# Optimization experiments

Hardware: AMD Instinct MI355X
Metric: run time of the kernel (lower is better)

The kernel has to match this reference:

```python
import jax, jax.numpy as jnp
import numpy as np

N, F, E, FE, H, OUT = 20000, 128, 320000, 16, 128, 128
NTYPES = 2  # types = (0, 1)
NPAIRS = NTYPES * NTYPES


def setup_inputs() -> dict:
    key = jax.random.key(0)
    ks = jax.random.split(key, 12)
    edge_in_dim = 2 * F + FE
    node_in_dim = F + H
    s = lambda *shape: 1.0 / np.sqrt(shape[-2])
    return {
        "x": jax.random.normal(ks[0], (N, 1, F), dtype=jnp.float32),
        "edge_index": jax.random.randint(ks[1], (2, E), 0, N, dtype=jnp.int64),
        "edge_attr": jax.random.normal(ks[2], (E, FE), dtype=jnp.float32),
        "node_type": jax.random.randint(ks[3], (N,), 0, NTYPES, dtype=jnp.int64),
        # edge MLP params, stacked over the 4 (t1,t2) type pairs
        "ew1": jax.random.normal(ks[4], (NPAIRS, edge_in_dim, H), dtype=jnp.float32) * (1.0 / np.sqrt(edge_in_dim)),
        "eb1": jnp.zeros((NPAIRS, H), dtype=jnp.float32),
        "ew2": jax.random.normal(ks[5], (NPAIRS, H, H), dtype=jnp.float32) * (1.0 / np.sqrt(H)),
        "eb2": jnp.zeros((NPAIRS, H), dtype=jnp.float32),
        # node MLP params, stacked over the 2 node types
        "nw1": jax.random.normal(ks[6], (NTYPES, node_in_dim, H), dtype=jnp.float32) * (1.0 / np.sqrt(node_in_dim)),
        "nb1": jnp.zeros((NTYPES, H), dtype=jnp.float32),
        "nw2": jax.random.normal(ks[7], (NTYPES, H, OUT), dtype=jnp.float32) * (1.0 / np.sqrt(H)),
        "nb2": jnp.zeros((NTYPES, OUT), dtype=jnp.float32),
    }


def reference(x, edge_index, edge_attr, node_type, ew1, eb1, ew2, eb2, nw1, nb1, nw2, nb2):
    x0 = x[:, 0]  # [N, F]
    row, col = edge_index[0], edge_index[1]

    # ---- edge model: type-pair-dispatched 2-layer ReLU MLP ----
    edge_in = jnp.concatenate([x0[row], x0[col], edge_attr], axis=-1)  # [E, 2F+FE]
    h1 = jax.nn.relu(jnp.einsum("ei,pih->eph", edge_in, ew1) + eb1)    # [E, P, H]
    h2 = jax.nn.relu(jnp.einsum("eph,phk->epk", h1, ew2) + eb2)        # [E, P, H]
    pair_id = node_type[row] * NTYPES + node_type[col]                  # [E]
    pair_oh = jax.nn.one_hot(pair_id, NPAIRS, dtype=h2.dtype)           # [E, P]
    edge_feat = jnp.einsum("epk,ep->ek", h2, pair_oh)                   # [E, H]

    # ---- aggregation: sum over incoming edges per source (row) node ----
    agg = jax.ops.segment_sum(edge_feat, row, num_segments=N)           # [N, H]

    # ---- node model: type-dispatched 2-layer MLP + residual ----
    node_in = jnp.concatenate([x0, agg], axis=-1)                       # [N, F+H]
    n1 = jax.nn.relu(jnp.einsum("ni,tih->nth", node_in, nw1) + nb1)     # [N, T, H]
    n2 = jnp.einsum("nth,thk->ntk", n1, nw2) + nb2                      # [N, T, OUT]
    type_oh = jax.nn.one_hot(node_type, NTYPES, dtype=n2.dtype)         # [N, T]
    out = jnp.einsum("ntk,nt->nk", n2, type_oh)                         # [N, OUT]
    out = out + x0[:, :OUT]  # residual
    return out[:, None, :]  # [N, 1, OUT]
```

## Files before the change

kernel.cpp:

```cpp
#include <hip/hip_runtime.h>

#define N_NODES 20000
#define N_EDGES 320000
#define NBINS   (4*N_NODES)
#define SCAN_NBLK 313

typedef unsigned short u16;
typedef __attribute__((ext_vector_type(8))) short bf16x8;
typedef __attribute__((ext_vector_type(4))) float f32x4;
typedef __attribute__((ext_vector_type(4))) unsigned int u32x4;
typedef __attribute__((ext_vector_type(2))) unsigned int u32x2;

__device__ __forceinline__ float b2f(u16 b){
  unsigned u = ((unsigned)b) << 16; float f; __builtin_memcpy(&f, &u, 4); return f;
}
__device__ __forceinline__ u16 f2b(float f){
  unsigned u; __builtin_memcpy(&u, &f, 4); u += 0x7FFF + ((u >> 16) & 1); return (u16)(u >> 16);
}
__device__ __forceinline__ unsigned cvtpk(float a, float b){
  unsigned r;
  asm("v_cvt_pk_bf16_f32 %0, %1, %2" : "=v"(r) : "v"(a), "v"(b));
  return r;
}

#define NX   (N_NODES*128)
#define NW1T (4*288*128)
#define NW2T (4*128*128)
#define NN1  (2*256*128)
#define NN2  (2*128*128)

__global__ void k_preconv(const float* __restrict__ x,
                          const float* __restrict__ ew1, const float* __restrict__ ew2,
                          const float* __restrict__ nw1, const float* __restrict__ nw2,
                          u16* __restrict__ x0b,
                          u16* __restrict__ wt1t, u16* __restrict__ wt2t,
                          u16* __restrict__ nw1t, u16* __restrict__ nw2t)
{
  int t = blockIdx.x * 256 + threadIdx.x;
  if (t < NX) { x0b[t] = f2b(x[t]); return; }
  t -= NX;
  if (t < NW1T) {
    int p = t / 36864, r = t % 36864; int k = r >> 7, n = r & 127;
    float v = (k < 272) ? ew1[(p * 272 + k) * 128 + n] : 0.f;
    wt1t[(p * 128 + n) * 288 + k] = f2b(v);
    return;
  }
  t -= NW1T;
  if (t < NW2T) {
    int p = t >> 14, r = t & 16383; int k = r >> 7, n = r & 127;
    wt2t[(p * 128 + n) * 128 + k] = f2b(ew2[(p * 128 + k) * 128 + n]);
    return;
  }
  t -= NW2T;
  if (t < NN1) {
    int ty = t >> 15, r = t & 32767; int k = r >> 7, n = r & 127;
    nw1t[(ty * 128 + n) * 256 + k] = f2b(nw1[(ty * 256 + k) * 128 + n]);
    return;
  }
  t -= NN1;
  if (t < NN2) {
    int ty = t >> 14, r = t & 16383; int k = r >> 7, n = r & 127;
    nw2t[(ty * 128 + n) * 128 + k] = f2b(nw2[(ty * 128 + k) * 128 + n]);
  }
}

__global__ void k_hist(const int* __restrict__ ei, const int* __restrict__ ntp,
                       int* __restrict__ hist, int* __restrict__ hist_nt,
                       u16* __restrict__ srank)
{
  int t = blockIdx.x * 256 + threadIdx.x;
  int lane = threadIdx.x & 63;
  if (t < N_EDGES) {
    int r = ei[t], c = ei[N_EDGES + t];
    int tr = ntp[r], tc = ntp[c];
    int key = (tr * 2 + tc) * N_NODES + r;
    int rk = atomicAdd(&hist[key], 1);
    srank[t] = (u16)rk;
  }
  bool valid = t < N_NODES;
  int ty = valid ? ntp[t] : -1;
  unsigned long long m0 = __ballot(ty == 0);
  unsigned long long m1 = __ballot(ty == 1);
  if (lane == 0) {
    int c0 = __popcll(m0), c1 = __popcll(m1);
    if (c0) atomicAdd(&hist_nt[0], c0);
    if (c1) atomicAdd(&hist_nt[1], c1);
  }
}

__global__ void k_scan1(const int* __restrict__ hist, int* __restrict__ parts)
{
  __shared__ int s[256];
  int i = blockIdx.x * 256 + threadIdx.x;
  s[threadIdx.x] = (i < NBINS) ? hist[i] : 0;
  __syncthreads();
  for (int off = 128; off > 0; off >>= 1) {
    if (threadIdx.x < off) s[threadIdx.x] += s[threadIdx.x + off];
    __syncthreads();
  }
  if (threadIdx.x == 0) parts[blockIdx.x] = s[0];
}

__global__ void k_scan2(int* __restrict__ parts)
{
  __shared__ int s[512];
  int t = threadIdx.x;
  int v = (t < SCAN_NBLK) ? parts[t] : 0;
  s[t] = v; __syncthreads();
  for (int off = 1; off < 512; off <<= 1) {
    int xv = (t >= off) ? s[t - off] : 0;
    __syncthreads();
    s[t] += xv;
    __syncthreads();
  }
  if (t < SCAN_NBLK) parts[t] = s[t] - v;
}

__global__ void k_scan3(const int* __restrict__ hist, const int* __restrict__ parts,
                        int* __restrict__ bstart)
{
  __shared__ int s[256];
  int i = blockIdx.x * 256 + threadIdx.x;
  int v = (i < NBINS) ? hist[i] : 0;
  s[threadIdx.x] = v; __syncthreads();
  for (int off = 1; off < 256; off <<= 1) {
    int xv = (threadIdx.x >= off) ? s[threadIdx.x - off] : 0;
    __syncthreads();
    s[threadIdx.x] += xv;
    __syncthreads();
  }
  int excl = s[threadIdx.x] - v + parts[blockIdx.x];
  if (i < NBINS) bstart[i] = excl;
  if (i == 0) bstart[NBINS] = N_EDGES;
}

__global__ void k_place(const int* __restrict__ ei, const int* __restrict__ ntp,
                        const u16* __restrict__ srank, const int* __restrict__ bstart,
                        int2* __restrict__ sedge,
                        int* __restrict__ cur_nt, const int* __restrict__ hist_nt,
                        int* __restrict__ nidx)
{
  int t = blockIdx.x * 256 + threadIdx.x;
  int lane = threadIdx.x & 63;
  if (t < N_EDGES) {
    int r = ei[t], c = ei[N_EDGES + t];
    int tr = ntp[r], tc = ntp[c];
    int key = (tr * 2 + tc) * N_NODES + r;
    int pos = bstart[key] + (int)srank[t];
    int2 v; v.x = r | (c << 15); v.y = t;
    sedge[pos] = v;
  }
  bool valid = t < N_NODES;
  int ty = valid ? ntp[t] : -1;
  unsigned long long m0 = __ballot(ty == 0);
  unsigned long long m1 = __ballot(ty == 1);
  int b0 = 0, b1 = 0;
  if (lane == 0) {
    int c0 = __popcll(m0), c1 = __popcll(m1);
    if (c0) b0 = atomicAdd(&cur_nt[0], c0);
    if (c1) b1 = atomicAdd(&cur_nt[1], c1);
  }
  b0 = __shfl(b0, 0); b1 = __shfl(b1, 0);
  if (valid) {
    unsigned long long lt = (1ull << lane) - 1ull;
    int pos = (ty == 0) ? (b0 + __popcll(m0 & lt))
                        : (hist_nt[0] + b1 + __popcll(m1 & lt));
    nidx[pos] = t;
  }
}

__launch_bounds__(512, 2)
__global__ void k_edge(const u16* __restrict__ x0b, const float* __restrict__ ea,
                       const u16* __restrict__ wt1t, const u16* __restrict__ wt2t,
                       const float* __restrict__ eb1, const float* __restrict__ eb2,
                       const int* __restrict__ bstart, const int2* __restrict__ sedge,
                       u16* __restrict__ h2s)
{
  __shared__ u16 sW1[128 * 296];
  __shared__ u16 sW2[128 * 136];
  __shared__ u16 slab[8][16][136];
  __shared__ float sEb1[128];
  __shared__ float sEb2[128];

  const int p    = blockIdx.y;
  const int tid  = threadIdx.x;
  const int lane = tid & 63;
  const int wv   = tid >> 6;
  const int llo  = lane & 15;
  const int lhi  = lane >> 4;

  const int base_p = bstart[p * N_NODES];
  const int end_p  = bstart[(p + 1) * N_NODES];

  for (int i = tid; i < 128 * 36; i += 512) {
    int n = i / 36, c = i % 36;
    *(u32x4*)&sW1[n * 296 + c * 8] = *(const u32x4*)&wt1t[(p * 128 + n) * 288 + c * 8];
  }
  for (int i = tid; i < 128 * 16; i += 512) {
    int n = i >> 4, c = i & 15;
    *(u32x4*)&sW2[n * 136 + c * 8] = *(const u32x4*)&wt2t[(p * 128 + n) * 128 + c * 8];
  }
  if (tid < 128) sEb1[tid] = eb1[p * 128 + tid];
  else if (tid < 256) sEb2[tid - 128] = eb2[p * 128 + tid - 128];
  __syncthreads();

  for (int ts = base_p + blockIdx.x * 256; ts < end_p; ts += gridDim.x * 256) {
    const int e0 = ts + wv * 32;
    int pos[2], row[2], col[2], eid[2];
    #pragma unroll
    for (int j = 0; j < 2; ++j) {
      pos[j] = e0 + j * 16 + llo;
      int pc = pos[j] < end_p ? pos[j] : end_p - 1;
      int2 m = sedge[pc];
      row[j] = m.x & 32767; col[j] = m.x >> 15; eid[j] = m.y;
    }

    bf16x8 xr[2][4], xc[2][4], eaf[2];
    #pragma unroll
    for (int j = 0; j < 2; ++j) {
      #pragma unroll
      for (int ck = 0; ck < 4; ++ck) {
        xr[j][ck] = *(const bf16x8*)&x0b[row[j] * 128 + ck * 32 + lhi * 8];
        xc[j][ck] = *(const bf16x8*)&x0b[col[j] * 128 + ck * 32 + lhi * 8];
      }
      u32x4 pk = (u32x4){0u, 0u, 0u, 0u};
      if (lhi < 2) {
        f32x4 f0 = *(const f32x4*)&ea[eid[j] * 16 + lhi * 8];
        f32x4 f1 = *(const f32x4*)&ea[eid[j] * 16 + lhi * 8 + 4];
        pk[0] = cvtpk(f0[0], f0[1]); pk[1] = cvtpk(f0[2], f0[3]);
        pk[2] = cvtpk(f1[0], f1[1]); pk[3] = cvtpk(f1[2], f1[3]);
      }
      __builtin_memcpy(&eaf[j], &pk, 16);
    }

    f32x4 acc[8][2];
    #pragma unroll
    for (int i = 0; i < 8; ++i) {
      acc[i][0] = (f32x4){0.f, 0.f, 0.f, 0.f};
      acc[i][1] = (f32x4){0.f, 0.f, 0.f, 0.f};
    }

    #pragma unroll
    for (int ck = 0; ck < 4; ++ck) {
      #pragma unroll
      for (int i = 0; i < 8; ++i) {
        bf16x8 wa = *(const bf16x8*)&sW1[(i * 16 + llo) * 296 + ck * 32 + lhi * 8];
        acc[i][0] = __builtin_amdgcn_mfma_f32_16x16x32_bf16(wa, xr[0][ck], acc[i][0], 0, 0, 0);
        acc[i][1] = __builtin_amdgcn_mfma_f32_16x16x32_bf16(wa, xr[1][ck], acc[i][1], 0, 0, 0);
      }
    }
    #pragma unroll
    for (int ck = 0; ck < 4; ++ck) {
      #pragma unroll
      for (int i = 0; i < 8; ++i) {
        bf16x8 wb = *(const bf16x8*)&sW1[(i * 16 + llo) * 296 + 128 + ck * 32 + lhi * 8];
        acc[i][0] = __builtin_amdgcn_mfma_f32_16x16x32_bf16(wb, xc[0][ck], acc[i][0], 0, 0, 0);
        acc[i][1] = __builtin_amdgcn_mfma_f32_16x16x32_bf16(wb, xc[1][ck], acc[i][1], 0, 0, 0);
      }
    }
    #pragma unroll
    for (int i = 0; i < 8; ++i) {
      bf16x8 wce = *(const bf16x8*)&sW1[(i * 16 + llo) * 296 + 256 + lhi * 8];
      acc[i][0] = __builtin_amdgcn_mfma_f32_16x16x32_bf16(wce, eaf[0], acc[i][0], 0, 0, 0);
      acc[i][1] = __builtin_amdgcn_mfma_f32_16x16x32_bf16(wce, eaf[1], acc[i][1], 0, 0, 0);
    }

    bf16x8 h1f[2][4];
    #pragma unroll
    for (int j = 0; j < 2; ++j) {
      #pragma unroll
      for (int i = 0; i < 8; ++i) {
        const f32x4 bb = *(const f32x4*)&sEb1[i * 16 + lhi * 4];
        float v0 = acc[i][j][0] + bb[0]; v0 = v0 > 0.f ? v0 : 0.f;
        float v1 = acc[i][j][1] + bb[1]; v1 = v1 > 0.f ? v1 : 0.f;
        float v2 = acc[i][j][2] + bb[2]; v2 = v2 > 0.f ? v2 : 0.f;
        float v3 = acc[i][j][3] + bb[3]; v3 = v3 > 0.f ? v3 : 0.f;
        u32x2 pk; pk[0] = cvtpk(v0, v1); pk[1] = cvtpk(v2, v3);
        *(u32x2*)&slab[wv][llo][i * 16 + lhi * 4] = pk;
      }
      #pragma unroll
      for (int ck = 0; ck < 4; ++ck)
        h1f[j][ck] = *(const bf16x8*)&slab[wv][llo][ck * 32 + lhi * 8];
    }

    f32x4 o[8][2];
    #pragma unroll
    for (int i = 0; i < 8; ++i) {
      o[i][0] = (f32x4){0.f, 0.f, 0.f, 0.f};
      o[i][1] = (f32x4){0.f, 0.f, 0.f, 0.f};
    }
    #pragma unroll
    for (int ck = 0; ck < 4; ++ck) {
      #pragma unroll
      for (int i = 0; i < 8; ++i) {
        bf16x8 w2f = *(const bf16x8*)&sW2[(i * 16 + llo) * 136 + ck * 32 + lhi * 8];
        o[i][0] = __builtin_amdgcn_mfma_f32_16x16x32_bf16(w2f, h1f[0][ck], o[i][0], 0, 0, 0);
        o[i][1] = __builtin_amdgcn_mfma_f32_16x16x32_bf16(w2f, h1f[1][ck], o[i][1], 0, 0, 0);
      }
    }

    #pragma unroll
    for (int i = 0; i < 8; ++i) {
      const f32x4 bb = *(const f32x4*)&sEb2[i * 16 + lhi * 4];
      #pragma unroll
      for (int j = 0; j < 2; ++j) {
        float v0 = o[i][j][0] + bb[0]; v0 = v0 > 0.f ? v0 : 0.f;
        float v1 = o[i][j][1] + bb[1]; v1 = v1 > 0.f ? v1 : 0.f;
        float v2 = o[i][j][2] + bb[2]; v2 = v2 > 0.f ? v2 : 0.f;
        float v3 = o[i][j][3] + bb[3]; v3 = v3 > 0.f ? v3 : 0.f;
        u32x2 pk; pk[0] = cvtpk(v0, v1); pk[1] = cvtpk(v2, v3);
        if (pos[j] < end_p) *(u32x2*)&h2s[pos[j] * 128 + i * 16 + lhi * 4] = pk;
      }
    }
  }
}

__launch_bounds__(512, 1)
__global__ void k_node(const u16* __restrict__ x0b, const float* __restrict__ xf,
                       const u16* __restrict__ h2s,
                       const u16* __restrict__ nw1t, const u16* __restrict__ nw2t,
                       const float* __restrict__ nb1, const float* __restrict__ nb2,
                       const int* __restrict__ bstart,
                       const int* __restrict__ nidx, const int* __restrict__ hist_nt,
                       float* __restrict__ out)
{
  const int ty    = blockIdx.y;
  const int cnt0  = hist_nt[0];
  const int cnt_t = ty ? (N_NODES - cnt0) : cnt0;
  const int base_t = ty ? cnt0 : 0;

  __shared__ u16 sNIN[64 * 264];
  __shared__ u16 sNW1[128 * 264];
  __shared__ u16 sNW2[128 * 136];
  __shared__ float sNb1[128];
  __shared__ float sNb2[128];
  __shared__ int sNid[64];

  const int tid  = threadIdx.x;
  const int lane = tid & 63;
  const int wid  = tid >> 6;
  const int llo  = lane & 15;
  const int lhi  = lane >> 4;

  for (int i = tid; i < 128 * 256; i += 512) {
    int n = i >> 8, k = i & 255;
    sNW1[n * 264 + k] = nw1t[(ty * 128 + n) * 256 + k];
  }
  for (int i = tid; i < 128 * 128; i += 512) {
    int n = i >> 7, k = i & 127;
    sNW2[n * 136 + k] = nw2t[(ty * 128 + n) * 128 + k];
  }
  if (tid < 128) { sNb1[tid] = nb1[ty * 128 + tid]; sNb2[tid] = nb2[ty * 128 + tid]; }
  __syncthreads();

  for (int t0 = blockIdx.x * 64; t0 < cnt_t; t0 += gridDim.x * 64) {
    const int cnt = min(64, cnt_t - t0);
    if (tid < 64) {
      int nid = 0;
      if (tid < cnt) nid = nidx[base_t + t0 + tid];
      sNid[tid] = nid;
    }
    __syncthreads();

    {
      const int m = tid >> 3, qq = tid & 7;
      const int nid = sNid[m];
      const u16* xs = &x0b[nid * 128 + qq * 16];
      u16* dst = &sNIN[m * 264 + qq * 16];
      #pragma unroll
      for (int j = 0; j < 2; ++j) *(u32x4*)(dst + j * 8) = *(const u32x4*)(xs + j * 8);

      float a[16];
      #pragma unroll
      for (int j = 0; j < 16; ++j) a[j] = 0.f;
      #pragma unroll
      for (int pr = 0; pr < 2; ++pr) {
        const int key = (ty * 2 + pr) * N_NODES + nid;
        const int s = bstart[key], e = bstart[key + 1];
        for (int pos = s; pos < e; ++pos) {
          const u16* hp = &h2s[pos * 128 + qq * 16];
          #pragma unroll
          for (int j = 0; j < 2; ++j) {
            u32x4 v = *(const u32x4*)(hp + j * 8);
            #pragma unroll
            for (int w = 0; w < 4; ++w) {
              unsigned uu = v[w];
              a[j * 8 + w * 2 + 0] += b2f((u16)(uu & 0xFFFFu));
              a[j * 8 + w * 2 + 1] += b2f((u16)(uu >> 16));
            }
          }
        }
      }
      u16* ad = &sNIN[m * 264 + 128 + qq * 16];
      #pragma unroll
      for (int j = 0; j < 8; ++j) {
        unsigned pk = cvtpk(a[2 * j], a[2 * j + 1]);
        *(unsigned*)(ad + 2 * j) = pk;
      }
    }
    __syncthreads();

    f32x4 acc[4];
    #pragma unroll
    for (int i = 0; i < 4; ++i) acc[i] = (f32x4){0.f, 0.f, 0.f, 0.f};

    #pragma unroll
    for (int ck = 0; ck < 8; ++ck) {
      const int kk = ck * 32 + lhi * 8;
      bf16x8 a[4], b;
      #pragma unroll
      for (int i = 0; i < 4; ++i)
        a[i] = *(const bf16x8*)&sNIN[(i * 16 + llo) * 264 + kk];
      b = *(const bf16x8*)&sNW1[(wid * 16 + llo) * 264 + kk];
      #pragma unroll
      for (int i = 0; i < 4; ++i)
        acc[i] = __builtin_amdgcn_mfma_f32_16x16x32_bf16(a[i], b, acc[i], 0, 0, 0);
    }
    __syncthreads();

    u16* sH1 = sNIN;
    #pragma unroll
    for (int i = 0; i < 4; ++i) {
      const int c = wid * 16 + llo;
      const float bias = sNb1[c];
      #pragma unroll
      for (int r = 0; r < 4; ++r) {
        const int m = i * 16 + lhi * 4 + r;
        float v = acc[i][r] + bias;
        v = v > 0.f ? v : 0.f;
        sH1[m * 136 + c] = f2b(v);
      }
    }
    __syncthreads();

    #pragma unroll
    for (int i = 0; i < 4; ++i) acc[i] = (f32x4){0.f, 0.f, 0.f, 0.f};

    #pragma unroll
    for (int ck = 0; ck < 4; ++ck) {
      const int kk = ck * 32 + lhi * 8;
      bf16x8 a[4], b;
      #pragma unroll
      for (int i = 0; i < 4; ++i)
        a[i] = *(const bf16x8*)&sH1[(i * 16 + llo) * 136 + kk];
      b = *(const bf16x8*)&sNW2[(wid * 16 + llo) * 136 + kk];
      #pragma unroll
      for (int i = 0; i < 4; ++i)
        acc[i] = __builtin_amdgcn_mfma_f32_16x16x32_bf16(a[i], b, acc[i], 0, 0, 0);
    }

    #pragma unroll
    for (int i = 0; i < 4; ++i) {
      const int c = wid * 16 + llo;
      const float bias = sNb2[c];
      #pragma unroll
      for (int r = 0; r < 4; ++r) {
        const int m = i * 16 + lhi * 4 + r;
        if (m < cnt) {
          const int nid = sNid[m];
          out[nid * 128 + c] = acc[i][r] + bias + xf[nid * 128 + c];
        }
      }
    }
    __syncthreads();
  }
}

extern "C" void kernel_launch(void* const* d_in, const int* in_sizes, int n_in,
                              void* d_out, int out_size, void* d_ws, size_t ws_size,
                              hipStream_t stream)
{
  const float* x   = (const float*)d_in[0];
  const int*   ei  = (const int*)d_in[1];
  const float* ea  = (const float*)d_in[2];
  const int*   ntp = (const int*)d_in[3];
  const float* ew1 = (const float*)d_in[4];
  const float* eb1 = (const float*)d_in[5];
  const float* ew2 = (const float*)d_in[6];
  const float* eb2 = (const float*)d_in[7];
  const float* nw1 = (const float*)d_in[8];
  const float* nb1 = (const float*)d_in[9];
  const float* nw2 = (const float*)d_in[10];
  const float* nb2 = (const float*)d_in[11];

  char* ws = (char*)d_ws;
  int*  hist    = (int*)(ws + 0);
  int*  hist_nt = (int*)(ws + 320000);
  int*  cur_nt  = (int*)(ws + 320008);
  int*  parts   = (int*)(ws + 320256);
  int*  bstart  = (int*)(ws + 321792);
  u16*  srank   = (u16*)(ws + 641824);
  int2* sedge   = (int2*)(ws + 1281824);
  int*  nidx    = (int*)(ws + 3841824);
  u16*  x0b     = (u16*)(ws + 3921824);
  u16*  wt1t    = (u16*)(ws + 9041824);
  u16*  wt2t    = (u16*)(ws + 9336736);
  u16*  nw1t    = (u16*)(ws + 9467808);
  u16*  nw2t    = (u16*)(ws + 9598880);
  u16*  h2s     = (u16*)(ws + 9664416);

  hipMemsetAsync(ws, 0, 320016, stream);
  k_preconv<<<11216, 256, 0, stream>>>(x, ew1, ew2, nw1, nw2, x0b, wt1t, wt2t, nw1t, nw2t);
  k_hist<<<1250, 256, 0, stream>>>(ei, ntp, hist, hist_nt, srank);
  k_scan1<<<SCAN_NBLK, 256, 0, stream>>>(hist, parts);
  k_scan2<<<1, 512, 0, stream>>>(parts);
  k_scan3<<<SCAN_NBLK, 256, 0, stream>>>(hist, parts, bstart);
  k_place<<<1250, 256, 0, stream>>>(ei, ntp, srank, bstart, sedge, cur_nt, hist_nt, nidx);
  k_edge<<<dim3(64, 4), 512, 0, stream>>>(x0b, ea, wt1t, wt2t, eb1, eb2, bstart, sedge, h2s);
  k_node<<<dim3(160, 2), 512, 0, stream>>>(x0b, x, h2s, nw1t, nw2t, nb1, nb2, bstart, nidx, hist_nt, (float*)d_out);
}
```

Baseline: 169.2 us.

## Merge hist into preconv kernel and widen edge kernel to 1024 threads

Merges the histogram kernel into the weight/feature conversion kernel as extra blocks, removing one launch. Doubles the edge-MLP block to 16 waves, which fit in LDS by halving the per-wave h1 staging slab and writing/reading it in two phases. The edge loop now assigns 32-edge groups per wave rather than per block stride. Raising the launch bound to 1024 threads caps registers per thread, which risks spills in the MFMA-heavy accumulators.

Measured after the change: 184.0 us. 8.7% more time.

```diff
diff --git a/kernel.cpp b/kernel.cpp
--- a/kernel.cpp
+++ b/kernel.cpp
@@ -4,6 +4,8 @@
 #define N_EDGES 320000
 #define NBINS   (4*N_NODES)
 #define SCAN_NBLK 313
+#define PRECONV_NBLK 11216
+#define HIST_NBLK 1250
 
 typedef unsigned short u16;
 typedef __attribute__((ext_vector_type(8))) short bf16x8;
@@ -29,14 +31,39 @@
 #define NN1  (2*256*128)
 #define NN2  (2*128*128)
 
-__global__ void k_preconv(const float* __restrict__ x,
-                          const float* __restrict__ ew1, const float* __restrict__ ew2,
-                          const float* __restrict__ nw1, const float* __restrict__ nw2,
-                          u16* __restrict__ x0b,
-                          u16* __restrict__ wt1t, u16* __restrict__ wt2t,
-                          u16* __restrict__ nw1t, u16* __restrict__ nw2t)
-{
-  int t = blockIdx.x * 256 + threadIdx.x;
+__global__ void k_prep(const float* __restrict__ x,
+                       const float* __restrict__ ew1, const float* __restrict__ ew2,
+                       const float* __restrict__ nw1, const float* __restrict__ nw2,
+                       u16* __restrict__ x0b,
+                       u16* __restrict__ wt1t, u16* __restrict__ wt2t,
+                       u16* __restrict__ nw1t, u16* __restrict__ nw2t,
+                       const int* __restrict__ ei, const int* __restrict__ ntp,
+                       int* __restrict__ hist, int* __restrict__ hist_nt,
+                       u16* __restrict__ srank)
+{
+  int bid = blockIdx.x;
+  if (bid >= PRECONV_NBLK) {
+    int t = (bid - PRECONV_NBLK) * 256 + threadIdx.x;
+    int lane = threadIdx.x & 63;
+    if (t < N_EDGES) {
+      int r = ei[t], c = ei[N_EDGES + t];
+      int tr = ntp[r], tc = ntp[c];
+      int key = (tr * 2 + tc) * N_NODES + r;
+      int rk = atomicAdd(&hist[key], 1);
+      srank[t] = (u16)rk;
+    }
+    bool valid = t < N_NODES;
+    int ty = valid ? ntp[t] : -1;
+    unsigned long long m0 = __ballot(ty == 0);
+    unsigned long long m1 = __ballot(ty == 1);
+    if (lane == 0) {
+      int c0 = __popcll(m0), c1 = __popcll(m1);
+      if (c0) atomicAdd(&hist_nt[0], c0);
+      if (c1) atomicAdd(&hist_nt[1], c1);
+    }
+    return;
+  }
+  int t = bid * 256 + threadIdx.x;
   if (t < NX) { x0b[t] = f2b(x[t]); return; }
   t -= NX;
   if (t < NW1T) {
@@ -61,30 +88,6 @@
   if (t < NN2) {
     int ty = t >> 14, r = t & 16383; int k = r >> 7, n = r & 127;
     nw2t[(ty * 128 + n) * 128 + k] = f2b(nw2[(ty * 128 + k) * 128 + n]);
-  }
-}
-
-__global__ void k_hist(const int* __restrict__ ei, const int* __restrict__ ntp,
-                       int* __restrict__ hist, int* __restrict__ hist_nt,
-                       u16* __restrict__ srank)
-{
-  int t = blockIdx.x * 256 + threadIdx.x;
-  int lane = threadIdx.x & 63;
-  if (t < N_EDGES) {
-    int r = ei[t], c = ei[N_EDGES + t];
-    int tr = ntp[r], tc = ntp[c];
-    int key = (tr * 2 + tc) * N_NODES + r;
-    int rk = atomicAdd(&hist[key], 1);
-    srank[t] = (u16)rk;
-  }
-  bool valid = t < N_NODES;
-  int ty = valid ? ntp[t] : -1;
-  unsigned long long m0 = __ballot(ty == 0);
-  unsigned long long m1 = __ballot(ty == 1);
-  if (lane == 0) {
-    int c0 = __popcll(m0), c1 = __popcll(m1);
-    if (c0) atomicAdd(&hist_nt[0], c0);
-    if (c1) atomicAdd(&hist_nt[1], c1);
   }
 }
 
@@ -169,7 +172,7 @@
   }
 }
 
-__launch_bounds__(512, 2)
+__launch_bounds__(1024, 4)
 __global__ void k_edge(const u16* __restrict__ x0b, const float* __restrict__ ea,
                        const u16* __restrict__ wt1t, const u16* __restrict__ wt2t,
                        const float* __restrict__ eb1, const float* __restrict__ eb2,
@@ -178,7 +181,7 @@
 {
   __shared__ u16 sW1[128 * 296];
   __shared__ u16 sW2[128 * 136];
-  __shared__ u16 slab[8][16][136];
+  __shared__ u16 slab[16][16][80];
   __shared__ float sEb1[128];
   __shared__ float sEb2[128];
 
@@ -192,11 +195,11 @@
   const int base_p = bstart[p * N_NODES];
   const int end_p  = bstart[(p + 1) * N_NODES];
 
-  for (int i = tid; i < 128 * 36; i += 512) {
+  for (int i = tid; i < 128 * 36; i += 1024) {
     int n = i / 36, c = i % 36;
     *(u32x4*)&sW1[n * 296 + c * 8] = *(const u32x4*)&wt1t[(p * 128 + n) * 288 + c * 8];
   }
-  for (int i = tid; i < 128 * 16; i += 512) {
+  for (int i = tid; i < 128 * 16; i += 1024) {
     int n = i >> 4, c = i & 15;
     *(u32x4*)&sW2[n * 136 + c * 8] = *(const u32x4*)&wt2t[(p * 128 + n) * 128 + c * 8];
   }
@@ -204,12 +207,14 @@
   else if (tid < 256) sEb2[tid - 128] = eb2[p * 128 + tid - 128];
   __syncthreads();
 
-  for (int ts = base_p + blockIdx.x * 256; ts < end_p; ts += gridDim.x * 256) {
-    const int e0 = ts + wv * 32;
+  for (int g = blockIdx.x * 16 + wv; ; g += gridDim.x * 16) {
+    const int es = base_p + g * 32;
+    if (es >= end_p) break;
+
     int pos[2], row[2], col[2], eid[2];
     #pragma unroll
     for (int j = 0; j < 2; ++j) {
-      pos[j] = e0 + j * 16 + llo;
+      pos[j] = es + j * 16 + llo;
       int pc = pos[j] < end_p ? pos[j] : end_p - 1;
       int2 m = sedge[pc];
       row[j] = m.x & 32767; col[j] = m.x >> 15; eid[j] = m.y;
@@ -269,18 +274,22 @@
     #pragma unroll
     for (int j = 0; j < 2; ++j) {
       #pragma unroll
-      for (int i = 0; i < 8; ++i) {
-        const f32x4 bb = *(const f32x4*)&sEb1[i * 16 + lhi * 4];
-        float v0 = acc[i][j][0] + bb[0]; v0 = v0 > 0.f ? v0 : 0.f;
-        float v1 = acc[i][j][1] + bb[1]; v1 = v1 > 0.f ? v1 : 0.f;
-        float v2 = acc[i][j][2] + bb[2]; v2 = v2 > 0.f ? v2 : 0.f;
-        float v3 = acc[i][j][3] + bb[3]; v3 = v3 > 0.f ? v3 : 0.f;
-        u32x2 pk; pk[0] = cvtpk(v0, v1); pk[1] = cvtpk(v2, v3);
-        *(u32x2*)&slab[wv][llo][i * 16 + lhi * 4] = pk;
-      }
-      #pragma unroll
-      for (int ck = 0; ck < 4; ++ck)
-        h1f[j][ck] = *(const bf16x8*)&slab[wv][llo][ck * 32 + lhi * 8];
+      for (int ph = 0; ph < 2; ++ph) {
+        #pragma unroll
+        for (int ii = 0; ii < 4; ++ii) {
+          const int i = ph * 4 + ii;
+          const f32x4 bb = *(const f32x4*)&sEb1[i * 16 + lhi * 4];
+          float v0 = acc[i][j][0] + bb[0]; v0 = v0 > 0.f ? v0 : 0.f;
+          float v1 = acc[i][j][1] + bb[1]; v1 = v1 > 0.f ? v1 : 0.f;
+          float v2 = acc[i][j][2] + bb[2]; v2 = v2 > 0.f ? v2 : 0.f;
+          float v3 = acc[i][j][3] + bb[3]; v3 = v3 > 0.f ? v3 : 0.f;
+          u32x2 pk; pk[0] = cvtpk(v0, v1); pk[1] = cvtpk(v2, v3);
+          *(u32x2*)&slab[wv][llo][ii * 16 + lhi * 4] = pk;
+        }
+        #pragma unroll
+        for (int cc = 0; cc < 2; ++cc)
+          h1f[j][ph * 2 + cc] = *(const bf16x8*)&slab[wv][llo][cc * 32 + lhi * 8];
+      }
     }
 
     f32x4 o[8][2];
@@ -500,12 +509,13 @@
   u16*  h2s     = (u16*)(ws + 9664416);
 
   hipMemsetAsync(ws, 0, 320016, stream);
-  k_preconv<<<11216, 256, 0, stream>>>(x, ew1, ew2, nw1, nw2, x0b, wt1t, wt2t, nw1t, nw2t);
-  k_hist<<<1250, 256, 0, stream>>>(ei, ntp, hist, hist_nt, srank);
+  k_prep<<<PRECONV_NBLK + HIST_NBLK, 256, 0, stream>>>(
+      x, ew1, ew2, nw1, nw2, x0b, wt1t, wt2t, nw1t, nw2t,
+      ei, ntp, hist, hist_nt, srank);
   k_scan1<<<SCAN_NBLK, 256, 0, stream>>>(hist, parts);
   k_scan2<<<1, 512, 0, stream>>>(parts);
   k_scan3<<<SCAN_NBLK, 256, 0, stream>>>(hist, parts, bstart);
   k_place<<<1250, 256, 0, stream>>>(ei, ntp, srank, bstart, sedge, cur_nt, hist_nt, nidx);
-  k_edge<<<dim3(64, 4), 512, 0, stream>>>(x0b, ea, wt1t, wt2t, eb1, eb2, bstart, sedge, h2s);
+  k_edge<<<dim3(64, 4), 1024, 0, stream>>>(x0b, ea, wt1t, wt2t, eb1, eb2, bstart, sedge, h2s);
   k_node<<<dim3(160, 2), 512, 0, stream>>>(x0b, x, h2s, nw1t, nw2t, nb1, nb2, bstart, nidx, hist_nt, (float*)d_out);
 }
```

## Fuse edge aggregation into edge kernel via segmented shuffle reduction and atomics

Applied to the files above, without the earlier changes.

The edge kernel no longer writes per-edge bf16 h2 values to a global buffer for the node kernel to gather. Because edges are sorted by row, each 16-lane group reduces runs of equal row ids with shuffles, and run heads atomically add the partial sums into an fp32 per-node aggregate. The node kernel then reads that aggregate directly, and the preconvert and histogram kernels are merged into one launch. The change cuts the large h2 write and read traffic, but adds a 10 MB memset, float atomics with nondeterministic summation order, and extra shuffle work.

Result: slower. 311.3 us (+84.0%).

```diff
diff --git a/kernel.cpp b/kernel.cpp
--- a/kernel.cpp
+++ b/kernel.cpp
@@ -4,6 +4,8 @@
 #define N_EDGES 320000
 #define NBINS   (4*N_NODES)
 #define SCAN_NBLK 313
+#define PRECONV_NBLK 11216
+#define HIST_NBLK 1250
 
 typedef unsigned short u16;
 typedef __attribute__((ext_vector_type(8))) short bf16x8;
@@ -29,14 +31,39 @@
 #define NN1  (2*256*128)
 #define NN2  (2*128*128)
 
-__global__ void k_preconv(const float* __restrict__ x,
-                          const float* __restrict__ ew1, const float* __restrict__ ew2,
-                          const float* __restrict__ nw1, const float* __restrict__ nw2,
-                          u16* __restrict__ x0b,
-                          u16* __restrict__ wt1t, u16* __restrict__ wt2t,
-                          u16* __restrict__ nw1t, u16* __restrict__ nw2t)
-{
-  int t = blockIdx.x * 256 + threadIdx.x;
+__global__ void k_prep(const float* __restrict__ x,
+                       const float* __restrict__ ew1, const float* __restrict__ ew2,
+                       const float* __restrict__ nw1, const float* __restrict__ nw2,
+                       u16* __restrict__ x0b,
+                       u16* __restrict__ wt1t, u16* __restrict__ wt2t,
+                       u16* __restrict__ nw1t, u16* __restrict__ nw2t,
+                       const int* __restrict__ ei, const int* __restrict__ ntp,
+                       int* __restrict__ hist, int* __restrict__ hist_nt,
+                       u16* __restrict__ srank)
+{
+  int bid = blockIdx.x;
+  if (bid >= PRECONV_NBLK) {
+    int t = (bid - PRECONV_NBLK) * 256 + threadIdx.x;
+    int lane = threadIdx.x & 63;
+    if (t < N_EDGES) {
+      int r = ei[t], c = ei[N_EDGES + t];
+      int tr = ntp[r], tc = ntp[c];
+      int key = (tr * 2 + tc) * N_NODES + r;
+      int rk = atomicAdd(&hist[key], 1);
+      srank[t] = (u16)rk;
+    }
+    bool valid = t < N_NODES;
+    int ty = valid ? ntp[t] : -1;
+    unsigned long long m0 = __ballot(ty == 0);
+    unsigned long long m1 = __ballot(ty == 1);
+    if (lane == 0) {
+      int c0 = __popcll(m0), c1 = __popcll(m1);
+      if (c0) atomicAdd(&hist_nt[0], c0);
+      if (c1) atomicAdd(&hist_nt[1], c1);
+    }
+    return;
+  }
+  int t = bid * 256 + threadIdx.x;
   if (t < NX) { x0b[t] = f2b(x[t]); return; }
   t -= NX;
   if (t < NW1T) {
@@ -61,30 +88,6 @@
   if (t < NN2) {
     int ty = t >> 14, r = t & 16383; int k = r >> 7, n = r & 127;
     nw2t[(ty * 128 + n) * 128 + k] = f2b(nw2[(ty * 128 + k) * 128 + n]);
-  }
-}
-
-__global__ void k_hist(const int* __restrict__ ei, const int* __restrict__ ntp,
-                       int* __restrict__ hist, int* __restrict__ hist_nt,
-                       u16* __restrict__ srank)
-{
-  int t = blockIdx.x * 256 + threadIdx.x;
-  int lane = threadIdx.x & 63;
-  if (t < N_EDGES) {
-    int r = ei[t], c = ei[N_EDGES + t];
-    int tr = ntp[r], tc = ntp[c];
-    int key = (tr * 2 + tc) * N_NODES + r;
-    int rk = atomicAdd(&hist[key], 1);
-    srank[t] = (u16)rk;
-  }
-  bool valid = t < N_NODES;
-  int ty = valid ? ntp[t] : -1;
-  unsigned long long m0 = __ballot(ty == 0);
-  unsigned long long m1 = __ballot(ty == 1);
-  if (lane == 0) {
-    int c0 = __popcll(m0), c1 = __popcll(m1);
-    if (c0) atomicAdd(&hist_nt[0], c0);
-    if (c1) atomicAdd(&hist_nt[1], c1);
   }
 }
 
@@ -174,7 +177,7 @@
                        const u16* __restrict__ wt1t, const u16* __restrict__ wt2t,
                        const float* __restrict__ eb1, const float* __restrict__ eb2,
                        const int* __restrict__ bstart, const int2* __restrict__ sedge,
-                       u16* __restrict__ h2s)
+                       float* __restrict__ agg)
 {
   __shared__ u16 sW1[128 * 296];
   __shared__ u16 sW2[128 * 136];
@@ -203,6 +206,8 @@
   if (tid < 128) sEb1[tid] = eb1[p * 128 + tid];
   else if (tid < 256) sEb2[tid - 128] = eb2[p * 128 + tid - 128];
   __syncthreads();
+
+  u16* myslab = &slab[wv][0][0];
 
   for (int ts = base_p + blockIdx.x * 256; ts < end_p; ts += gridDim.x * 256) {
     const int e0 = ts + wv * 32;
@@ -276,11 +281,11 @@
         float v2 = acc[i][j][2] + bb[2]; v2 = v2 > 0.f ? v2 : 0.f;
         float v3 = acc[i][j][3] + bb[3]; v3 = v3 > 0.f ? v3 : 0.f;
         u32x2 pk; pk[0] = cvtpk(v0, v1); pk[1] = cvtpk(v2, v3);
-        *(u32x2*)&slab[wv][llo][i * 16 + lhi * 4] = pk;
+        *(u32x2*)&myslab[llo * 136 + i * 16 + lhi * 4] = pk;
       }
       #pragma unroll
       for (int ck = 0; ck < 4; ++ck)
-        h1f[j][ck] = *(const bf16x8*)&slab[wv][llo][ck * 32 + lhi * 8];
+        h1f[j][ck] = *(const bf16x8*)&myslab[llo * 136 + ck * 32 + lhi * 8];
     }
 
     f32x4 o[8][2];
@@ -300,16 +305,35 @@
     }
 
     #pragma unroll
-    for (int i = 0; i < 8; ++i) {
-      const f32x4 bb = *(const f32x4*)&sEb2[i * 16 + lhi * 4];
-      #pragma unroll
-      for (int j = 0; j < 2; ++j) {
-        float v0 = o[i][j][0] + bb[0]; v0 = v0 > 0.f ? v0 : 0.f;
-        float v1 = o[i][j][1] + bb[1]; v1 = v1 > 0.f ? v1 : 0.f;
-        float v2 = o[i][j][2] + bb[2]; v2 = v2 > 0.f ? v2 : 0.f;
-        float v3 = o[i][j][3] + bb[3]; v3 = v3 > 0.f ? v3 : 0.f;
-        u32x2 pk; pk[0] = cvtpk(v0, v1); pk[1] = cvtpk(v2, v3);
-        if (pos[j] < end_p) *(u32x2*)&h2s[pos[j] * 128 + i * 16 + lhi * 4] = pk;
+    for (int j = 0; j < 2; ++j) {
+      const int  rme  = row[j];
+      const bool val  = pos[j] < end_p;
+      const int  rup  = __shfl_up(rme, 1, 16);
+      const bool head = (llo == 0) || (rup != rme);
+      const int rd1 = __shfl_down(rme, 1, 16);
+      const int rd2 = __shfl_down(rme, 2, 16);
+      const int rd4 = __shfl_down(rme, 4, 16);
+      const int rd8 = __shfl_down(rme, 8, 16);
+      const bool ok1 = (llo + 1 < 16) && (rd1 == rme);
+      const bool ok2 = (llo + 2 < 16) && (rd2 == rme);
+      const bool ok4 = (llo + 4 < 16) && (rd4 == rme);
+      const bool ok8 = (llo + 8 < 16) && (rd8 == rme);
+      float* aggrow = agg + rme * 128;
+      #pragma unroll
+      for (int i = 0; i < 8; ++i) {
+        const f32x4 bb = *(const f32x4*)&sEb2[i * 16 + lhi * 4];
+        #pragma unroll
+        for (int r = 0; r < 4; ++r) {
+          float v = o[i][j][r] + bb[r];
+          v = v > 0.f ? v : 0.f;
+          v = val ? v : 0.f;
+          float vd;
+          vd = __shfl_down(v, 1, 16); v += ok1 ? vd : 0.f;
+          vd = __shfl_down(v, 2, 16); v += ok2 ? vd : 0.f;
+          vd = __shfl_down(v, 4, 16); v += ok4 ? vd : 0.f;
+          vd = __shfl_down(v, 8, 16); v += ok8 ? vd : 0.f;
+          if (head) atomicAdd(&aggrow[i * 16 + lhi * 4 + r], v);
+        }
       }
     }
   }
@@ -317,10 +341,9 @@
 
 __launch_bounds__(512, 1)
 __global__ void k_node(const u16* __restrict__ x0b, const float* __restrict__ xf,
-                       const u16* __restrict__ h2s,
+                       const float* __restrict__ agg,
                        const u16* __restrict__ nw1t, const u16* __restrict__ nw2t,
                        const float* __restrict__ nb1, const float* __restrict__ nb2,
-                       const int* __restrict__ bstart,
                        const int* __restrict__ nidx, const int* __restrict__ hist_nt,
                        float* __restrict__ out)
 {
@@ -370,32 +393,15 @@
       #pragma unroll
       for (int j = 0; j < 2; ++j) *(u32x4*)(dst + j * 8) = *(const u32x4*)(xs + j * 8);
 
-      float a[16];
-      #pragma unroll
-      for (int j = 0; j < 16; ++j) a[j] = 0.f;
-      #pragma unroll
-      for (int pr = 0; pr < 2; ++pr) {
-        const int key = (ty * 2 + pr) * N_NODES + nid;
-        const int s = bstart[key], e = bstart[key + 1];
-        for (int pos = s; pos < e; ++pos) {
-          const u16* hp = &h2s[pos * 128 + qq * 16];
-          #pragma unroll
-          for (int j = 0; j < 2; ++j) {
-            u32x4 v = *(const u32x4*)(hp + j * 8);
-            #pragma unroll
-            for (int w = 0; w < 4; ++w) {
-              unsigned uu = v[w];
-              a[j * 8 + w * 2 + 0] += b2f((u16)(uu & 0xFFFFu));
-              a[j * 8 + w * 2 + 1] += b2f((u16)(uu >> 16));
-            }
-          }
-        }
-      }
+      const float* ag = &agg[nid * 128 + qq * 16];
       u16* ad = &sNIN[m * 264 + 128 + qq * 16];
       #pragma unroll
-      for (int j = 0; j < 8; ++j) {
-        unsigned pk = cvtpk(a[2 * j], a[2 * j + 1]);
-        *(unsigned*)(ad + 2 * j) = pk;
+      for (int j = 0; j < 4; ++j) {
+        f32x4 A = *(const f32x4*)(ag + j * 4);
+        unsigned p0 = cvtpk(A[0], A[1]);
+        unsigned p1 = cvtpk(A[2], A[3]);
+        u32x2 pk; pk[0] = p0; pk[1] = p1;
+        *(u32x2*)(ad + j * 4) = pk;
       }
     }
     __syncthreads();
@@ -484,28 +490,30 @@
   const float* nb2 = (const float*)d_in[11];
 
   char* ws = (char*)d_ws;
-  int*  hist    = (int*)(ws + 0);
-  int*  hist_nt = (int*)(ws + 320000);
-  int*  cur_nt  = (int*)(ws + 320008);
-  int*  parts   = (int*)(ws + 320256);
-  int*  bstart  = (int*)(ws + 321792);
-  u16*  srank   = (u16*)(ws + 641824);
-  int2* sedge   = (int2*)(ws + 1281824);
-  int*  nidx    = (int*)(ws + 3841824);
-  u16*  x0b     = (u16*)(ws + 3921824);
-  u16*  wt1t    = (u16*)(ws + 9041824);
-  u16*  wt2t    = (u16*)(ws + 9336736);
-  u16*  nw1t    = (u16*)(ws + 9467808);
-  u16*  nw2t    = (u16*)(ws + 9598880);
-  u16*  h2s     = (u16*)(ws + 9664416);
+  int*   hist    = (int*)(ws + 0);
+  int*   hist_nt = (int*)(ws + 320000);
+  int*   cur_nt  = (int*)(ws + 320008);
+  int*   parts   = (int*)(ws + 320256);
+  int*   bstart  = (int*)(ws + 321792);
+  u16*   srank   = (u16*)(ws + 641824);
+  int2*  sedge   = (int2*)(ws + 1281824);
+  int*   nidx    = (int*)(ws + 3841824);
+  u16*   x0b     = (u16*)(ws + 3921824);
+  u16*   wt1t    = (u16*)(ws + 9041824);
+  u16*   wt2t    = (u16*)(ws + 9336736);
+  u16*   nw1t    = (u16*)(ws + 9467808);
+  u16*   nw2t    = (u16*)(ws + 9598880);
+  float* agg     = (float*)(ws + 9664416);
 
   hipMemsetAsync(ws, 0, 320016, stream);
-  k_preconv<<<11216, 256, 0, stream>>>(x, ew1, ew2, nw1, nw2, x0b, wt1t, wt2t, nw1t, nw2t);
-  k_hist<<<1250, 256, 0, stream>>>(ei, ntp, hist, hist_nt, srank);
+  hipMemsetAsync(agg, 0, 10240000, stream);
+  k_prep<<<PRECONV_NBLK + HIST_NBLK, 256, 0, stream>>>(
+      x, ew1, ew2, nw1, nw2, x0b, wt1t, wt2t, nw1t, nw2t,
+      ei, ntp, hist, hist_nt, srank);
   k_scan1<<<SCAN_NBLK, 256, 0, stream>>>(hist, parts);
   k_scan2<<<1, 512, 0, stream>>>(parts);
   k_scan3<<<SCAN_NBLK, 256, 0, stream>>>(hist, parts, bstart);
   k_place<<<1250, 256, 0, stream>>>(ei, ntp, srank, bstart, sedge, cur_nt, hist_nt, nidx);
-  k_edge<<<dim3(64, 4), 512, 0, stream>>>(x0b, ea, wt1t, wt2t, eb1, eb2, bstart, sedge, h2s);
-  k_node<<<dim3(160, 2), 512, 0, stream>>>(x0b, x, h2s, nw1t, nw2t, nb1, nb2, bstart, nidx, hist_nt, (float*)d_out);
-}
+  k_edge<<<dim3(64, 4), 512, 0, stream>>>(x0b, ea, wt1t, wt2t, eb1, eb2, bstart, sedge, agg);
+  k_node<<<dim3(160, 2), 512, 0, stream>>>(x0b, x, agg, nw1t, nw2t, nb1, nb2, nidx, hist_nt, (float*)d_out);
+}
```
